# Performance work log

Measured on AMD Instinct MI355X. Metric: run time of the kernel, lower is better.

## Reference

```python
import jax, jax.numpy as jnp
import numpy as np

N = 400_000   # units (atoms)
C = 4         # n_channel
A = 3         # n_axis
D = 128       # d_hidden
NBLK = 50_000 # blocks
B = 64        # batches (static segment count)
NR = 16       # n_rbf
CUT = 7.0     # cutoff
LN_EPS = 1e-5


def radial_basis(d):
    # GemNet-style: polynomial envelope (exponent 5) * Gaussian basis on d/cutoff
    ds = d / CUT
    env = 1.0 - 21.0 * ds**5 + 35.0 * ds**6 - 15.0 * ds**7
    env = jnp.where(ds < 1.0, env, 0.0)
    offsets = jnp.linspace(0.0, 1.0, NR)
    coeff = -0.5 / (offsets[1] - offsets[0]) ** 2
    g = jnp.exp(coeff * (ds[:, None] - offsets[None, :]) ** 2)  # [M, NR]
    return env[:, None] * g


def setup_inputs() -> dict:
    key = jax.random.key(0)
    ks = jax.random.split(key, 8)
    H = jax.random.normal(ks[0], (N, D), jnp.float32)
    Z = jax.random.normal(ks[1], (N, C, A), jnp.float32)
    block_id = jnp.sort(jax.random.randint(ks[2], (N,), 0, NBLK))
    batch_id = jnp.sort(jax.random.randint(ks[3], (NBLK,), 0, B))
    sigma = jnp.ones((1, C, 1), jnp.float32)
    W1 = jax.random.normal(ks[4], (C * NR, D), jnp.float32) / np.sqrt(C * NR)
    b1 = jnp.zeros((D,), jnp.float32)
    W2 = jax.random.normal(ks[5], (D, D), jnp.float32) / np.sqrt(D)
    b2 = jnp.zeros((D,), jnp.float32)
    ln_w = jnp.ones((D,), jnp.float32)
    ln_b = jnp.zeros((D,), jnp.float32)
    return {"H": H, "Z": Z, "sigma": sigma, "W1": W1, "b1": b1, "W2": W2,
            "b2": b2, "ln_w": ln_w, "ln_b": ln_b,
            "block_id": block_id, "batch_id": batch_id}


def reference(H, Z, sigma, W1, b1, W2, b2, ln_w, ln_b, block_id, batch_id):
    uid = batch_id[block_id]                                  # [N]
    cnt = jax.ops.segment_sum(jnp.ones((N,), jnp.float32), uid, num_segments=B)
    cnt_safe = jnp.maximum(cnt, 1.0)

    # scatter_mean(Z, uid) -> per-batch centroid [B, C, A]
    Zsum = jax.ops.segment_sum(Z.reshape(N, C * A), uid, num_segments=B)
    Z_c = (Zsum / cnt_safe[:, None]).reshape(B, C, A)
    Z_cg = Z_c[uid]                                           # [N, C, A]
    Z_cent = Z - Z_cg

    # scatter_std over (units x axes) per channel, unbiased
    src = jnp.swapaxes(Z_cent, 1, 2).reshape(N * A, C)        # [N*A, C]
    idx3 = jnp.repeat(uid, A)                                 # [N*A]
    cnt3 = cnt * A
    mean_s = jax.ops.segment_sum(src, idx3, num_segments=B) / jnp.maximum(cnt3, 1.0)[:, None]
    sq = jax.ops.segment_sum((src - mean_s[idx3]) ** 2, idx3, num_segments=B)
    var = sq / jnp.maximum(cnt3 - 1.0, 1.0)[:, None]
    std = jnp.sqrt(var)                                       # [B, C]

    rescale = (1.0 / std)[:, :, None] * sigma                 # [B, C, 1]
    Z_out = Z_cg + Z_cent * rescale[uid]

    rbf = radial_basis(rescale.reshape(-1)).reshape(B, C * NR)  # [B, C*NR]
    h = jax.nn.silu(rbf @ W1 + b1)
    h = jax.nn.silu(h @ W2 + b2)                              # [B, D]

    Hn = H + h[uid]
    mu = jnp.mean(Hn, axis=-1, keepdims=True)
    v = jnp.var(Hn, axis=-1, keepdims=True)
    H_out = (Hn - mu) * jax.lax.rsqrt(v + LN_EPS) * ln_w + ln_b
    return (H_out, Z_out, rescale)
```

## Files before the change

### kernel.cpp

```cpp
#include <hip/hip_runtime.h>
#include <hip/hip_bf16.h>

#define N_ATOMS 400000
#define BATCHES 64
#define DH 128

#define ACC_OFF 0
#define ZC_OFF  1088
#define RS_OFF  1856
#define HB_OFF  2112
#define UID_OFF 10304

typedef float f4 __attribute__((ext_vector_type(4)));

__device__ __forceinline__ f4 ntload4(const f4* p) { return __builtin_nontemporal_load(p); }
__device__ __forceinline__ float silu_f(float x) { return x / (1.f + expf(-x)); }

__global__ __launch_bounds__(256) void k1_stats(
    const float* __restrict__ Z, const int* __restrict__ block_id,
    const int* __restrict__ batch_id, float* __restrict__ acc,
    unsigned char* __restrict__ uid8) {
  __shared__ float bins[BATCHES * 17];
  for (int i = threadIdx.x; i < BATCHES * 17; i += 256) bins[i] = 0.f;
  __syncthreads();

  const f4* Z4 = (const f4*)Z;
  int n = blockIdx.x * 256 + threadIdx.x;
  bool valid = (n < N_ATOMS);
  int uid = -1;
  float z[12];
#pragma unroll
  for (int j = 0; j < 12; ++j) z[j] = 0.f;
  if (valid) {
    uid = batch_id[block_id[n]];
    uid8[n] = (unsigned char)uid;
    f4 a = Z4[n * 3 + 0];
    f4 b = Z4[n * 3 + 1];
    f4 c = Z4[n * 3 + 2];
    z[0] = a.x; z[1] = a.y; z[2]  = a.z; z[3]  = a.w;
    z[4] = b.x; z[5] = b.y; z[6]  = b.z; z[7]  = b.w;
    z[8] = c.x; z[9] = c.y; z[10] = c.z; z[11] = c.w;
  }

  int lo = valid ? uid : 0x7fffffff;
  int hi = uid;
#pragma unroll
  for (int m = 32; m; m >>= 1) {
    lo = min(lo, __shfl_xor(lo, m));
    hi = max(hi, __shfl_xor(hi, m));
  }

  if (lo == hi) {
    float vals[16];
#pragma unroll
    for (int j = 0; j < 12; ++j) vals[j] = z[j];
#pragma unroll
    for (int c = 0; c < 4; ++c)
      vals[12 + c] = z[c*3]*z[c*3] + z[c*3+1]*z[c*3+1] + z[c*3+2]*z[c*3+2];
#pragma unroll
    for (int v = 0; v < 16; ++v) {
      float x = vals[v];
#pragma unroll
      for (int m = 32; m; m >>= 1) x += __shfl_xor(x, m);
      vals[v] = x;
    }
    unsigned long long mb = __ballot(valid);
    if ((threadIdx.x & 63) == 0) {
      atomicAdd(&bins[hi * 17 + 0], (float)__popcll(mb));
#pragma unroll
      for (int v = 0; v < 16; ++v) atomicAdd(&bins[hi * 17 + 1 + v], vals[v]);
    }
  } else if (hi >= 0) {
    if (valid) {
      atomicAdd(&bins[uid * 17 + 0], 1.f);
#pragma unroll
      for (int j = 0; j < 12; ++j) atomicAdd(&bins[uid * 17 + 1 + j], z[j]);
#pragma unroll
      for (int c = 0; c < 4; ++c)
        atomicAdd(&bins[uid * 17 + 13 + c],
                  z[c*3]*z[c*3] + z[c*3+1]*z[c*3+1] + z[c*3+2]*z[c*3+2]);
    }
  }
  __syncthreads();
  for (int i = threadIdx.x; i < BATCHES * 17; i += 256) {
    float v = bins[i];
    if (v != 0.f) atomicAdd(&acc[i], v);
  }
}

__global__ __launch_bounds__(128) void k2_mlp(
    const float* __restrict__ sigma, const float* __restrict__ W1,
    const float* __restrict__ b1, const float* __restrict__ W2,
    const float* __restrict__ b2, const float* __restrict__ acc,
    float* __restrict__ Zc, float* __restrict__ resc,
    float* __restrict__ hbuf, float* __restrict__ resc_out) {
  int b = blockIdx.x, t = threadIdx.x;
  __shared__ float rbf_s[64];
  __shared__ float h1_s[128];
  __shared__ float resc_s[4];

  if (t < 4) {
    int c = t;
    float cnt = acc[b * 17];
    float cs = fmaxf(cnt, 1.f);
    float s2 = 0.f;
#pragma unroll
    for (int a = 0; a < 3; ++a) {
      float zc = acc[b * 17 + 1 + c * 3 + a] / cs;
      Zc[b * 12 + c * 3 + a] = zc;
      s2 += zc * zc;
    }
    float sq = acc[b * 17 + 13 + c] - cnt * s2;
    float denom = fmaxf(cnt * 3.f - 1.f, 1.f);
    float var = fmaxf(sq / denom, 0.f);
    float r = sigma[c] / sqrtf(var);
    resc_s[c] = r;
    resc[b * 4 + c] = r;
    resc_out[b * 4 + c] = r;
  }
  __syncthreads();
  if (t < 64) {
    int c = t >> 4, ri = t & 15;
    float ds = resc_s[c] * (1.f / 7.f);
    float env = 0.f;
    if (ds < 1.f) {
      float d2 = ds * ds;
      float d5 = d2 * d2 * ds;
      env = 1.f - 21.f * d5 + 35.f * d5 * ds - 15.f * d5 * d2;
    }
    float off = (float)ri * (1.f / 15.f);
    float dd = ds - off;
    rbf_s[t] = env * expf(-112.5f * dd * dd);
  }
  __syncthreads();
  float s = b1[t];
#pragma unroll 8
  for (int k = 0; k < 64; ++k) s += rbf_s[k] * W1[k * 128 + t];
  h1_s[t] = silu_f(s);
  __syncthreads();
  float s2 = b2[t];
#pragma unroll 8
  for (int k = 0; k < 128; ++k) s2 += h1_s[k] * W2[k * 128 + t];
  hbuf[b * 128 + t] = silu_f(s2);
}

__global__ __launch_bounds__(256) void k3_apply(
    const float* __restrict__ H, const float* __restrict__ Z,
    const unsigned char* __restrict__ uid8,
    const float* __restrict__ ln_w, const float* __restrict__ ln_b,
    const float* __restrict__ Zc, const float* __restrict__ resc,
    const float* __restrict__ hbuf,
    float* __restrict__ Hout, float* __restrict__ Zout) {
  int t = threadIdx.x;
  int sub = t >> 4, l = t & 15;
  int base = blockIdx.x * 64;
  int n0 = base + sub * 4;

  unsigned int u4 = *(const unsigned int*)&uid8[n0];
  int uid[4] = {(int)(u4 & 0xff), (int)((u4 >> 8) & 0xff),
                (int)((u4 >> 16) & 0xff), (int)(u4 >> 24)};

  const f4* H4 = (const f4*)H;
  const f4* HB4 = (const f4*)hbuf;

  f4 va[4], vb[4];
#pragma unroll
  for (int a = 0; a < 4; ++a) {
    size_t r = (size_t)(n0 + a) * 32;
    va[a] = ntload4(&H4[r + l]);
    vb[a] = ntload4(&H4[r + 16 + l]);
  }
  f4 xa[4], xb[4];
#pragma unroll
  for (int a = 0; a < 4; ++a) {
    xa[a] = va[a] + HB4[uid[a] * 32 + l];
    xb[a] = vb[a] + HB4[uid[a] * 32 + 16 + l];
  }

  float s[4], q[4];
#pragma unroll
  for (int a = 0; a < 4; ++a) {
    s[a] = (xa[a].x + xa[a].y + xa[a].z + xa[a].w)
         + (xb[a].x + xb[a].y + xb[a].z + xb[a].w);
    q[a] = (xa[a].x*xa[a].x + xa[a].y*xa[a].y + xa[a].z*xa[a].z + xa[a].w*xa[a].w)
         + (xb[a].x*xb[a].x + xb[a].y*xb[a].y + xb[a].z*xb[a].z + xb[a].w*xb[a].w);
  }
#pragma unroll
  for (int m = 1; m < 16; m <<= 1) {
#pragma unroll
    for (int a = 0; a < 4; ++a) {
      s[a] += __shfl_xor(s[a], m);
      q[a] += __shfl_xor(q[a], m);
    }
  }

  const f4* LW4 = (const f4*)ln_w;
  const f4* LB4 = (const f4*)ln_b;
  f4 w0 = LW4[l], w1 = LW4[16 + l];
  f4 bb0 = LB4[l], bb1 = LB4[16 + l];

  f4* HO4 = (f4*)Hout;
#pragma unroll
  for (int a = 0; a < 4; ++a) {
    float mean = s[a] * (1.f / 128.f);
    float inv = rsqrtf(q[a] * (1.f / 128.f) - mean * mean + 1e-5f);
    size_t r = (size_t)(n0 + a) * 32;
    f4 o;
    o.x = (xa[a].x - mean) * inv * w0.x + bb0.x;
    o.y = (xa[a].y - mean) * inv * w0.y + bb0.y;
    o.z = (xa[a].z - mean) * inv * w0.z + bb0.z;
    o.w = (xa[a].w - mean) * inv * w0.w + bb0.w;
    HO4[r + l] = o;
    o.x = (xb[a].x - mean) * inv * w1.x + bb1.x;
    o.y = (xb[a].y - mean) * inv * w1.y + bb1.y;
    o.z = (xb[a].z - mean) * inv * w1.z + bb1.z;
    o.w = (xb[a].w - mean) * inv * w1.w + bb1.w;
    HO4[r + 16 + l] = o;
  }

  if (t < 192) {
    int atom = base + t / 3;
    int comp = t - (t / 3) * 3;
    int zuid = uid8[atom];
    const f4* Z4 = (const f4*)Z;
    f4 z = Z4[atom * 3 + comp];
    float zz[4] = {z.x, z.y, z.z, z.w};
    float oo[4];
#pragma unroll
    for (int k = 0; k < 4; ++k) {
      int j = comp * 4 + k;
      int c = j / 3;
      float zcv = Zc[zuid * 12 + j];
      float r = resc[zuid * 4 + c];
      oo[k] = zcv + (zz[k] - zcv) * r;
    }
    f4 ov = {oo[0], oo[1], oo[2], oo[3]};
    ((f4*)Zout)[atom * 3 + comp] = ov;
  }
}

extern "C" void kernel_launch(void* const* d_in, const int* in_sizes, int n_in,
                              void* d_out, int out_size, void* d_ws, size_t ws_size,
                              hipStream_t stream) {
  const float* H     = (const float*)d_in[0];
  const float* Z     = (const float*)d_in[1];
  const float* sigma = (const float*)d_in[2];
  const float* W1    = (const float*)d_in[3];
  const float* b1    = (const float*)d_in[4];
  const float* W2    = (const float*)d_in[5];
  const float* b2    = (const float*)d_in[6];
  const float* ln_w  = (const float*)d_in[7];
  const float* ln_b  = (const float*)d_in[8];
  const int* block_id = (const int*)d_in[9];
  const int* batch_id = (const int*)d_in[10];

  float* ws   = (float*)d_ws;
  float* acc  = ws + ACC_OFF;
  float* Zc   = ws + ZC_OFF;
  float* resc = ws + RS_OFF;
  float* hbuf = ws + HB_OFF;
  unsigned char* uid8 = (unsigned char*)(ws + UID_OFF);

  float* Hout = (float*)d_out;
  float* Zout = Hout + (size_t)N_ATOMS * DH;
  float* resc_out = Zout + (size_t)N_ATOMS * 12;

  hipMemsetAsync(acc, 0, BATCHES * 17 * sizeof(float), stream);
  k1_stats<<<(N_ATOMS + 255) / 256, 256, 0, stream>>>(Z, block_id, batch_id, acc, uid8);
  k2_mlp<<<BATCHES, 128, 0, stream>>>(sigma, W1, b1, W2, b2, acc, Zc, resc, hbuf, resc_out);
  k3_apply<<<N_ATOMS / 64, 256, 0, stream>>>(H, Z, uid8, ln_w, ln_b,
                                             Zc, resc, hbuf, Hout, Zout);
}
```

Measured before the change: 103.2 us.

## Replace global atomic stats accumulation with per-block partials reduced in MLP kernel

The stats kernel now uses 512-thread blocks and, instead of atomically adding every shared bin into a global accumulator, writes at most two batch bins per block (min and max uid) plus a header. The MLP kernel scans all block headers and reduces the matching partials for its batch. This removes the memset launch and global atomic contention, but assumes each 512-atom block spans at most two batches (relies on sorted ids and batch sizes larger than a block), and adds a serial scan over 782 partials in each MLP block.

```diff
diff --git a/kernel.cpp b/kernel.cpp
--- a/kernel.cpp
+++ b/kernel.cpp
@@ -4,28 +4,32 @@
 #define N_ATOMS 400000
 #define BATCHES 64
 #define DH 128
-
-#define ACC_OFF 0
-#define ZC_OFF  1088
-#define RS_OFF  1856
-#define HB_OFF  2112
-#define UID_OFF 10304
+#define NB1 782
+
+#define PART_OFF 0
+#define HDR_OFF  26588
+#define ZC_OFF   28160
+#define RS_OFF   28928
+#define HB_OFF   29184
+#define UID_OFF  37376
 
 typedef float f4 __attribute__((ext_vector_type(4)));
 
 __device__ __forceinline__ f4 ntload4(const f4* p) { return __builtin_nontemporal_load(p); }
 __device__ __forceinline__ float silu_f(float x) { return x / (1.f + expf(-x)); }
 
-__global__ __launch_bounds__(256) void k1_stats(
+__global__ __launch_bounds__(512) void k1_stats(
     const float* __restrict__ Z, const int* __restrict__ block_id,
-    const int* __restrict__ batch_id, float* __restrict__ acc,
-    unsigned char* __restrict__ uid8) {
+    const int* __restrict__ batch_id, float* __restrict__ partials,
+    int* __restrict__ hdr, unsigned char* __restrict__ uid8) {
   __shared__ float bins[BATCHES * 17];
-  for (int i = threadIdx.x; i < BATCHES * 17; i += 256) bins[i] = 0.f;
+  __shared__ int smin, smax;
+  for (int i = threadIdx.x; i < BATCHES * 17; i += 512) bins[i] = 0.f;
+  if (threadIdx.x == 0) { smin = 1 << 30; smax = -1; }
   __syncthreads();
 
   const f4* Z4 = (const f4*)Z;
-  int n = blockIdx.x * 256 + threadIdx.x;
+  int n = blockIdx.x * 512 + threadIdx.x;
   bool valid = (n < N_ATOMS);
   int uid = -1;
   float z[12];
@@ -81,36 +85,77 @@
                   z[c*3]*z[c*3] + z[c*3+1]*z[c*3+1] + z[c*3+2]*z[c*3+2]);
     }
   }
-  __syncthreads();
-  for (int i = threadIdx.x; i < BATCHES * 17; i += 256) {
-    float v = bins[i];
-    if (v != 0.f) atomicAdd(&acc[i], v);
+  if ((threadIdx.x & 63) == 0 && hi >= 0) {
+    atomicMin(&smin, lo);
+    atomicMax(&smax, hi);
+  }
+  __syncthreads();
+
+  int blo = smin, bhi = smax;
+  if (threadIdx.x < 17) {
+    partials[blockIdx.x * 34 + threadIdx.x] = bins[blo * 17 + threadIdx.x];
+  } else if (threadIdx.x < 34) {
+    int i = threadIdx.x - 17;
+    partials[blockIdx.x * 34 + threadIdx.x] = (bhi > blo) ? bins[bhi * 17 + i] : 0.f;
+  } else if (threadIdx.x == 34) {
+    hdr[blockIdx.x * 2 + 0] = blo;
+    hdr[blockIdx.x * 2 + 1] = (bhi > blo) ? bhi : -1;
   }
 }
 
 __global__ __launch_bounds__(128) void k2_mlp(
     const float* __restrict__ sigma, const float* __restrict__ W1,
     const float* __restrict__ b1, const float* __restrict__ W2,
-    const float* __restrict__ b2, const float* __restrict__ acc,
+    const float* __restrict__ b2,
+    const float* __restrict__ partials, const int* __restrict__ hdr,
     float* __restrict__ Zc, float* __restrict__ resc,
     float* __restrict__ hbuf, float* __restrict__ resc_out) {
   int b = blockIdx.x, t = threadIdx.x;
+  __shared__ float sbins[17];
   __shared__ float rbf_s[64];
   __shared__ float h1_s[128];
   __shared__ float resc_s[4];
 
+  if (t < 17) sbins[t] = 0.f;
+  __syncthreads();
+
+  {
+    float local[17];
+#pragma unroll
+    for (int i = 0; i < 17; ++i) local[i] = 0.f;
+    bool touched = false;
+    for (int r = t; r < NB1; r += 128) {
+      int lo = hdr[r * 2], hi = hdr[r * 2 + 1];
+      if (lo == b) {
+        touched = true;
+#pragma unroll
+        for (int i = 0; i < 17; ++i) local[i] += partials[r * 34 + i];
+      }
+      if (hi == b) {
+        touched = true;
+#pragma unroll
+        for (int i = 0; i < 17; ++i) local[i] += partials[r * 34 + 17 + i];
+      }
+    }
+    if (touched) {
+#pragma unroll
+      for (int i = 0; i < 17; ++i) atomicAdd(&sbins[i], local[i]);
+    }
+  }
+  __syncthreads();
+
   if (t < 4) {
     int c = t;
-    float cnt = acc[b * 17];
+    float cnt = sbins[0];
     float cs = fmaxf(cnt, 1.f);
     float s2 = 0.f;
 #pragma unroll
     for (int a = 0; a < 3; ++a) {
-      float zc = acc[b * 17 + 1 + c * 3 + a] / cs;
+      float zc = sbins[1 + c * 3 + a] / cs;
       Zc[b * 12 + c * 3 + a] = zc;
       s2 += zc * zc;
     }
-    float sq = acc[b * 17 + 13 + c] - cnt * s2;
+    float sq = sbins[13 + c] - cnt * s2;
     float denom = fmaxf(cnt * 3.f - 1.f, 1.f);
     float var = fmaxf(sq / denom, 0.f);
     float r = sigma[c] / sqrtf(var);
@@ -254,20 +299,21 @@
   const int* block_id = (const int*)d_in[9];
   const int* batch_id = (const int*)d_in[10];
 
-  float* ws   = (float*)d_ws;
-  float* acc  = ws + ACC_OFF;
-  float* Zc   = ws + ZC_OFF;
-  float* resc = ws + RS_OFF;
-  float* hbuf = ws + HB_OFF;
+  float* ws       = (float*)d_ws;
+  float* partials = ws + PART_OFF;
+  int*   hdr      = (int*)(ws + HDR_OFF);
+  float* Zc       = ws + ZC_OFF;
+  float* resc     = ws + RS_OFF;
+  float* hbuf     = ws + HB_OFF;
   unsigned char* uid8 = (unsigned char*)(ws + UID_OFF);
 
   float* Hout = (float*)d_out;
   float* Zout = Hout + (size_t)N_ATOMS * DH;
   float* resc_out = Zout + (size_t)N_ATOMS * 12;
 
-  hipMemsetAsync(acc, 0, BATCHES * 17 * sizeof(float), stream);
-  k1_stats<<<(N_ATOMS + 255) / 256, 256, 0, stream>>>(Z, block_id, batch_id, acc, uid8);
-  k2_mlp<<<BATCHES, 128, 0, stream>>>(sigma, W1, b1, W2, b2, acc, Zc, resc, hbuf, resc_out);
+  k1_stats<<<NB1, 512, 0, stream>>>(Z, block_id, batch_id, partials, hdr, uid8);
+  k2_mlp<<<BATCHES, 128, 0, stream>>>(sigma, W1, b1, W2, b2, partials, hdr,
+                                      Zc, resc, hbuf, resc_out);
   k3_apply<<<N_ATOMS / 64, 256, 0, stream>>>(H, Z, uid8, ln_w, ln_b,
                                              Zc, resc, hbuf, Hout, Zout);
 }
```

After: 108.2 us. +4.8%, slower.
